# Performance work log

Measured on AMD Instinct MI355X. Metric: run time of the kernel, lower is better.

## Reference

```python
import jax, jax.numpy as jnp
import numpy as np
from jax.ops import segment_sum, segment_max

N, H, E, NEXP, K, L, HEADS, NM = 384, 768, 12288, 8, 2, 3, 4, 38
GAMMA, LAMBDA_SPD = 2.0, 0.5


def _ln(x, g, b, eps=1e-5):
    m = jnp.mean(x, -1, keepdims=True)
    v = jnp.mean((x - m) ** 2, -1, keepdims=True)
    return (x - m) / jnp.sqrt(v + eps) * g + b


def _gelu(x):
    return jax.nn.gelu(x, approximate=False)


def setup_inputs() -> dict:
    key = jax.random.key(0)
    ks = jax.random.split(key, 20)
    r = lambda i, sh: jax.random.normal(ks[i], sh, jnp.float32) * 0.02
    z = lambda sh: jnp.zeros(sh, jnp.float32)
    o = lambda sh: jnp.ones(sh, jnp.float32)
    return dict(
        feat_text=jax.random.normal(ks[0], (N, H), jnp.float32),
        feat_image=jax.random.normal(ks[1], (N, H), jnp.float32),
        spd_matrix=jax.random.uniform(ks[2], (N, N), dtype=jnp.float32),
        src=jax.random.randint(ks[3], (E,), 0, N, jnp.int32),
        dst=jax.random.randint(ks[4], (E,), 0, N, jnp.int32),
        mask_idx=jax.random.randint(ks[5], (NM,), 0, N, jnp.int32),
        mask_token=r(6, (H,)),
        gate_W=r(7, (H, NEXP)), gate_b=z((NEXP,)),
        exp_W1=r(8, (NEXP, H, H)), exp_b1=z((NEXP, H)),
        exp_g1=o((NEXP, H)), exp_be1=z((NEXP, H)),
        exp_W2=r(9, (NEXP, H, H)), exp_b2=z((NEXP, H)),
        gat_W=r(10, (L, H, HEADS * H)), gat_al=r(11, (L, HEADS, H)),
        gat_ar=r(12, (L, HEADS, H)), gat_b=z((L, HEADS * H)),
        dec_W1=r(13, (2, H, H)), dec_b1=z((2, H)),
        dec_g=o((2, H)), dec_be=z((2, H)),
        dec_W2=r(14, (2, H, H)), dec_b2=z((2, H)),
        spd_W1=r(15, (2 * H, H)), spd_b1=z((H,)),
        spd_g=o((H,)), spd_be=z((H,)),
        spd_W2=r(16, (H, 1)), spd_b2=z((1,)),
    )


def _forward(feat_text, feat_image, spd_matrix, mask_token, gate_W, gate_b,
             exp_W1, exp_b1, exp_g1, exp_be1, exp_W2, exp_b2,
             gat_W, gat_al, gat_ar, gat_b,
             dec_W1, dec_b1, dec_g, dec_be, dec_W2, dec_b2,
             spd_W1, spd_b1, spd_g, spd_be, spd_W2, spd_b2,
             src, dst, mask_idx):
    # mean of domain features, then mask-token replacement at fixed indices
    x = (feat_text + feat_image) * 0.5
    xm = x.at[mask_idx].set(mask_token)

    # --- MoE (all experts computed densely, top-2 gathered, as in source) ---
    gw = jax.nn.softmax(xm @ gate_W + gate_b, axis=-1)              # [N,NEXP]
    topw, topi = jax.lax.top_k(gw, K)
    topw = topw / jnp.sum(topw, -1, keepdims=True)
    eh = _gelu(_ln(jnp.einsum('nd,edh->neh', xm, exp_W1) + exp_b1, exp_g1, exp_be1))
    eo = jnp.einsum('neh,ehk->nek', eh, exp_W2) + exp_b2            # [N,NEXP,H]
    sel = jnp.take_along_axis(eo, topi[:, :, None], axis=1)          # [N,K,H]
    h = jnp.sum(sel * topw[:, :, None], axis=1)                      # [N,H]

    # --- stacked GATConv layers (DGL semantics), head-mean after each ---
    for l in range(L):
        f = (h @ gat_W[l]).reshape(N, HEADS, H)                      # [N,heads,H]
        el = jnp.sum(f * gat_al[l], -1)                              # [N,heads]
        er = jnp.sum(f * gat_ar[l], -1)
        e = jax.nn.leaky_relu(el[src] + er[dst], 0.2)                # [E,heads]
        emax = segment_max(e, dst, num_segments=N)
        emax = jnp.where(jnp.isfinite(emax), emax, 0.0)
        ex = jnp.exp(e - emax[dst])
        den = segment_sum(ex, dst, num_segments=N)
        alpha = ex / jnp.maximum(den[dst], 1e-9)                     # edge softmax by dst
        rst = segment_sum(alpha[:, :, None] * f[src], dst, num_segments=N)
        h = jnp.mean(rst + gat_b[l].reshape(HEADS, H), axis=1)       # [N,H]

    # --- domain reconstruction loss on masked nodes ---
    hm = h[mask_idx]
    feats = (feat_text, feat_image)
    recon = jnp.float32(0.0)
    for d in range(2):
        zz = _gelu(_ln(hm @ dec_W1[d] + dec_b1[d], dec_g[d], dec_be[d]))
        rec = zz @ dec_W2[d] + dec_b2[d]
        orig = feats[d][mask_idx]
        denom = jnp.maximum(jnp.linalg.norm(rec, axis=-1) * jnp.linalg.norm(orig, axis=-1), 1e-8)
        cos = jnp.sum(rec * orig, -1) / denom
        recon = recon + jnp.mean((1.0 - cos) ** GAMMA)

    # --- SPD loss over all N^2 pairs, vectorized ---
    # concat([h_i, h_j]) @ W1 == h_i @ W1[:H] + h_j @ W1[H:]  (exact decomposition)
    pa = h @ spd_W1[:H]                                              # [N,H]
    pb = h @ spd_W1[H:]                                              # [N,H]
    zp = _gelu(_ln(pa[:, None, :] + pb[None, :, :] + spd_b1, spd_g, spd_be))  # [N,N,H]
    pred = (zp @ spd_W2)[..., 0] + spd_b2[0]                         # [N,N]
    spd_loss = jnp.mean((pred - spd_matrix) ** 2)

    total = recon + LAMBDA_SPD * spd_loss
    return total, h


def reference(feat_text, feat_image, spd_matrix, src, dst, mask_idx, mask_token,
              gate_W, gate_b, exp_W1, exp_b1, exp_g1, exp_be1, exp_W2, exp_b2,
              gat_W, gat_al, gat_ar, gat_b,
              dec_W1, dec_b1, dec_g, dec_be, dec_W2, dec_b2,
              spd_W1, spd_b1, spd_g, spd_be, spd_W2, spd_b2):
    return _forward(feat_text, feat_image, spd_matrix, mask_token, gate_W, gate_b,
                    exp_W1, exp_b1, exp_g1, exp_be1, exp_W2, exp_b2,
                    gat_W, gat_al, gat_ar, gat_b,
                    dec_W1, dec_b1, dec_g, dec_be, dec_W2, dec_b2,
                    spd_W1, spd_b1, spd_g, spd_be, spd_W2, spd_b2,
                    src, dst, mask_idx)
```

## Files before the change

kernel.cpp:

```cpp
#include <hip/hip_runtime.h>
#include <hip/hip_bf16.h>
#include <math.h>

#define NN 384
#define HD 768
#define EE 12288
#define NCHUNK (EE / 256)
#define NEXPERT 8
#define TOPK 2
#define NLAYER 3
#define NHEADS 4
#define NMASK 38

typedef __attribute__((ext_vector_type(8))) short short8v;
typedef __attribute__((ext_vector_type(4))) float f32x4;
typedef __attribute__((ext_vector_type(2))) float f32x2;
typedef __attribute__((ext_vector_type(4))) int int4v;

__device__ __forceinline__ float gelu_f(float x) {
    return x * 0.5f * (1.f + erff(x * 0.70710678118654752440f));
}

__device__ __forceinline__ ushort f2bf(float x) {
    unsigned u = __float_as_uint(x);
    u += 0x7fffu + ((u >> 16) & 1u);
    return (ushort)(u >> 16);
}

__global__ __launch_bounds__(256) void k_xm_gate(const float* __restrict__ a,
        const float* __restrict__ b, const int* __restrict__ mask_idx,
        const float* __restrict__ mt, ushort* __restrict__ xm_bf,
        const float* __restrict__ gW, const float* __restrict__ gb,
        int* __restrict__ topi, float* __restrict__ topw) {
    int n = blockIdx.x, tid = threadIdx.x;
    __shared__ float xs[HD];
    __shared__ int ism;
    __shared__ float logits[NEXPERT];
    if (tid == 0) ism = 0;
    __syncthreads();
    if (tid < NMASK && mask_idx[tid] == n) ism = 1;
    __syncthreads();
#pragma unroll
    for (int r = 0; r < 3; r++) {
        int j = r * 256 + tid;
        float v = ism ? mt[j] : 0.5f * (a[(size_t)n * HD + j] + b[(size_t)n * HD + j]);
        xs[j] = v;
        xm_bf[(size_t)n * HD + j] = f2bf(v);
    }
    __syncthreads();
    int grp = tid >> 5;
    int l32 = tid & 31;
    float p = 0.f;
    for (int dd = l32; dd < HD; dd += 32) p += xs[dd] * gW[dd * NEXPERT + grp];
#pragma unroll
    for (int m = 1; m < 32; m <<= 1) p += __shfl_xor(p, m, 32);
    if (l32 == 0) logits[grp] = p + gb[grp];
    __syncthreads();
    if (tid == 0) {
        float mx = logits[0];
#pragma unroll
        for (int e = 1; e < NEXPERT; e++) mx = fmaxf(mx, logits[e]);
        float sm[NEXPERT]; float s = 0.f;
#pragma unroll
        for (int e = 0; e < NEXPERT; e++) { sm[e] = expf(logits[e] - mx); s += sm[e]; }
#pragma unroll
        for (int e = 0; e < NEXPERT; e++) sm[e] /= s;
        int i0 = 0; float b0 = sm[0];
#pragma unroll
        for (int e = 1; e < NEXPERT; e++) if (sm[e] > b0) { b0 = sm[e]; i0 = e; }
        int i1 = -1; float b1v = -1.f;
#pragma unroll
        for (int e = 0; e < NEXPERT; e++) if (e != i0 && sm[e] > b1v) { b1v = sm[e]; i1 = e; }
        float ssum = b0 + b1v;
        topi[n * 2] = i0; topi[n * 2 + 1] = i1;
        topw[n * 2] = b0 / ssum; topw[n * 2 + 1] = b1v / ssum;
    }
}

__global__ __launch_bounds__(256) void k_transpose_all(
        const float* __restrict__ w1, const float* __restrict__ w2,
        const float* __restrict__ gw, const float* __restrict__ sw,
        const float* __restrict__ dw1, const float* __restrict__ dw2,
        ushort* __restrict__ o1, ushort* __restrict__ o2, ushort* __restrict__ og,
        ushort* __restrict__ os, ushort* __restrict__ od1, ushort* __restrict__ od2) {
    int b = blockIdx.x;
    const float* src; ushort* dst; int N, loc, tilesX;
    if (b < 4608)       { src = w1;  dst = o1;  N = HD;     loc = b;         tilesX = 24; }
    else if (b < 9216)  { src = w2;  dst = o2;  N = HD;     loc = b - 4608;  tilesX = 24; }
    else if (b < 16128) { src = gw;  dst = og;  N = 4 * HD; loc = b - 9216;  tilesX = 96; }
    else if (b < 17280) { src = sw;  dst = os;  N = HD;     loc = b - 16128; tilesX = 24; }
    else if (b < 18432) { src = dw1; dst = od1; N = HD;     loc = b - 17280; tilesX = 24; }
    else                { src = dw2; dst = od2; N = HD;     loc = b - 18432; tilesX = 24; }
    const int K = HD;
    int tilesPerZ = tilesX * 24;
    int z = loc / tilesPerZ;
    int rem = loc - z * tilesPerZ;
    int ty = rem / tilesX, tx = rem - ty * tilesX;
    const float* inz = src + (size_t)z * K * N;
    ushort* outz = dst + (size_t)z * K * N;
    int n0 = tx * 32, k0 = ty * 32;

    __shared__ float t[32][36];
    int r = threadIdx.x >> 3, c4 = (threadIdx.x & 7) * 4;
    float4 v = *reinterpret_cast<const float4*>(inz + (size_t)(k0 + r) * N + n0 + c4);
    t[r][c4] = v.x; t[r][c4 + 1] = v.y; t[r][c4 + 2] = v.z; t[r][c4 + 3] = v.w;
    __syncthreads();
    int orow = n0 + r;
    uint2 p;
    ushort b0 = f2bf(t[c4 + 0][r]);
    ushort b1 = f2bf(t[c4 + 1][r]);
    ushort b2 = f2bf(t[c4 + 2][r]);
    ushort b3 = f2bf(t[c4 + 3][r]);
    p.x = (unsigned)b0 | ((unsigned)b1 << 16);
    p.y = (unsigned)b2 | ((unsigned)b3 << 16);
    *reinterpret_cast<uint2*>(outz + (size_t)orow * K + k0 + c4) = p;
}

__global__ __launch_bounds__(256) void k_moe_meta(const int* __restrict__ topi,
        int* __restrict__ ecnt, int* __restrict__ estart, int* __restrict__ posArr,
        int* __restrict__ eofpos, int* __restrict__ rowlist, int* __restrict__ dec_rs) {
    __shared__ int ti[NN * TOPK];
    __shared__ int cnt[NEXPERT];
    __shared__ int est[NEXPERT + 1];
    int tid = threadIdx.x;
    if (tid < NEXPERT) cnt[tid] = 0;
    __syncthreads();
    for (int a = tid; a < NN * TOPK; a += 256) ti[a] = topi[a];
    __syncthreads();
    for (int a = tid; a < NN * TOPK; a += 256) atomicAdd(&cnt[ti[a]], 1);
    __syncthreads();
    if (tid == 0) {
        int s = 0;
        for (int e = 0; e < NEXPERT; e++) { est[e] = s; s += cnt[e]; }
        est[NEXPERT] = s;
        dec_rs[0] = 0; dec_rs[1] = NMASK;
    }
    __syncthreads();
    if (tid < NEXPERT) { ecnt[tid] = cnt[tid]; estart[tid] = est[tid]; }
    if (tid == 0) estart[NEXPERT] = est[NEXPERT];
    for (int a = tid; a < NN * TOPK; a += 256) {
        int e = ti[a]; int rank = 0;
        for (int a2 = 0; a2 < a; a2++) rank += (ti[a2] == e) ? 1 : 0;
        int p = est[e] + rank;
        posArr[a] = p; eofpos[p] = e; rowlist[p] = a >> 1;
    }
}

__global__ __launch_bounds__(256) void k_hist(const int* __restrict__ dst,
                                              int* __restrict__ counts) {
    __shared__ int h[NN];
    int c = blockIdx.x;
    for (int i = threadIdx.x; i < NN; i += 256) h[i] = 0;
    __syncthreads();
    atomicAdd(&h[dst[c * 256 + threadIdx.x]], 1);
    __syncthreads();
    for (int i = threadIdx.x; i < NN; i += 256) counts[c * NN + i] = h[i];
}

__global__ __launch_bounds__(NN) void k_scan_all(const int* __restrict__ counts,
        int* __restrict__ chunkbase, int* __restrict__ nstart) {
    __shared__ int tot[NN];
    int n = threadIdx.x;
    int s = 0;
    for (int c = 0; c < NCHUNK; c++) { chunkbase[c * NN + n] = s; s += counts[c * NN + n]; }
    tot[n] = s;
    __syncthreads();
    for (int off = 1; off < NN; off <<= 1) {
        int v = tot[n];
        int add = (n >= off) ? tot[n - off] : 0;
        __syncthreads();
        tot[n] = v + add;
        __syncthreads();
    }
    nstart[n + 1] = tot[n];
    if (n == 0) nstart[0] = 0;
}

__global__ __launch_bounds__(256) void k_rank2(const int* __restrict__ dst,
        const int* __restrict__ chunkbase, const int* __restrict__ nstart,
        int* __restrict__ esorted) {
    __shared__ int ds[256];
    int c = blockIdx.x;
    int e = c * 256 + threadIdx.x;
    int d = dst[e];
    ds[threadIdx.x] = d;
    __syncthreads();
    int r = 0;
    for (int i = 0; i < threadIdx.x; i++) r += (ds[i] == d) ? 1 : 0;
    esorted[nstart[d] + chunkbase[c * NN + d] + r] = e;
}

__device__ __forceinline__ short8v ldfrag(const ushort* s, int r, int kb) {
    int c = kb ^ (r & 7);
    return *reinterpret_cast<const short8v*>(s + r * 64 + c * 8);
}

__global__ __launch_bounds__(256) void k_mfma_gemm(
        const ushort* __restrict__ A, const ushort* __restrict__ Bt, float* __restrict__ C,
        int M, int K, int lda, int ldc, long strideBt, long strideC,
        const int* __restrict__ rowsA, const int* __restrict__ Ms,
        const int* __restrict__ rowStarts) {
    int z = blockIdx.z;
    int Meff = Ms ? Ms[z] : M;
    int row0 = blockIdx.y * 64;
    if (row0 >= Meff) return;
    int col0 = blockIdx.x * 64;
    int rowbase = rowStarts ? rowStarts[z] : 0;
    const ushort* Btz = Bt + (size_t)z * strideBt;
    float* Cz = C + (size_t)rowbase * ldc + (size_t)z * strideC;
    const int* rz = rowsA ? (rowsA + rowbase) : nullptr;

    __shared__ ushort Asm[64 * 64];
    __shared__ ushort Bsm[64 * 64];

    int tid = threadIdx.x;
    int w = tid >> 6, lane = tid & 63;
    int wr = w >> 1, wc = w & 1;
    int l15 = lane & 15, lq = lane >> 4;

    f32x4 acc[2][2];
#pragma unroll
    for (int i = 0; i < 2; i++)
#pragma unroll
        for (int j = 0; j < 2; j++) acc[i][j] = (f32x4){0.f, 0.f, 0.f, 0.f};

    for (int k0 = 0; k0 < K; k0 += 64) {
#pragma unroll
        for (int ii = 0; ii < 2; ii++) {
            int i = tid + ii * 256;
            int r = i >> 3, c = i & 7;
            int cs = c ^ (r & 7);
            int4v av = (int4v){0, 0, 0, 0};
            int grow = row0 + r;
            if (grow < Meff) {
                int srow = rz ? rz[grow] : (rowbase + grow);
                av = *reinterpret_cast<const int4v*>(A + (size_t)srow * lda + k0 + c * 8);
            }
            *reinterpret_cast<int4v*>(&Asm[r * 64 + cs * 8]) = av;
            int4v bv = *reinterpret_cast<const int4v*>(Btz + (size_t)(col0 + r) * K + k0 + c * 8);
            *reinterpret_cast<int4v*>(&Bsm[r * 64 + cs * 8]) = bv;
        }
        __syncthreads();
#pragma unroll
        for (int ks = 0; ks < 2; ks++) {
            int kb = ks * 4 + lq;
            short8v a0 = ldfrag(Asm, wr * 32 + l15, kb);
            short8v a1 = ldfrag(Asm, wr * 32 + 16 + l15, kb);
            short8v b0 = ldfrag(Bsm, wc * 32 + l15, kb);
            short8v b1 = ldfrag(Bsm, wc * 32 + 16 + l15, kb);
            acc[0][0] = __builtin_amdgcn_mfma_f32_16x16x32_bf16(a0, b0, acc[0][0], 0, 0, 0);
            acc[0][1] = __builtin_amdgcn_mfma_f32_16x16x32_bf16(a0, b1, acc[0][1], 0, 0, 0);
            acc[1][0] = __builtin_amdgcn_mfma_f32_16x16x32_bf16(a1, b0, acc[1][0], 0, 0, 0);
            acc[1][1] = __builtin_amdgcn_mfma_f32_16x16x32_bf16(a1, b1, acc[1][1], 0, 0, 0);
        }
        __syncthreads();
    }
#pragma unroll
    for (int ai = 0; ai < 2; ai++)
#pragma unroll
        for (int bi = 0; bi < 2; bi++) {
            int rbase = row0 + wr * 32 + ai * 16 + (lq << 2);
            int cc = col0 + wc * 32 + bi * 16 + l15;
#pragma unroll
            for (int r = 0; r < 4; r++) {
                int rr = rbase + r;
                if (rr < Meff) Cz[(size_t)rr * ldc + cc] = acc[ai][bi][r];
            }
        }
}

__global__ __launch_bounds__(256) void k_ln_gelu(const float* __restrict__ t1,
        ushort* __restrict__ ehb, const float* __restrict__ b1, const float* __restrict__ g,
        const float* __restrict__ be, const int* __restrict__ eofpos) {
    int row = blockIdx.x;
    int e = eofpos[row];
    int tid = threadIdx.x;
    __shared__ float rA[4], rB[4];
    float v[3]; float s1 = 0.f, s2 = 0.f;
#pragma unroll
    for (int r = 0; r < 3; r++) {
        int c = r * 256 + tid;
        float x = t1[(size_t)row * HD + c] + b1[e * HD + c];
        v[r] = x; s1 += x; s2 += x * x;
    }
#pragma unroll
    for (int m = 1; m < 64; m <<= 1) { s1 += __shfl_xor(s1, m); s2 += __shfl_xor(s2, m); }
    int wave = tid >> 6, lane = tid & 63;
    if (lane == 0) { rA[wave] = s1; rB[wave] = s2; }
    __syncthreads();
    float S1 = rA[0] + rA[1] + rA[2] + rA[3];
    float S2 = rB[0] + rB[1] + rB[2] + rB[3];
    float mean = S1 * (1.f / HD);
    float var = S2 * (1.f / HD) - mean * mean;
    float rstd = rsqrtf(var + 1e-5f);
#pragma unroll
    for (int r = 0; r < 3; r++) {
        int c = r * 256 + tid;
        float zn = (v[r] - mean) * rstd * g[e * HD + c] + be[e * HD + c];
        ehb[(size_t)row * HD + c] = f2bf(gelu_f(zn));
    }
}

__global__ void k_combine_moe(const float* __restrict__ eo, const float* __restrict__ b2,
        const int* __restrict__ topi, const float* __restrict__ topw,
        const int* __restrict__ posArr, float* __restrict__ h, ushort* __restrict__ hb) {
    int n = blockIdx.x;
    int tid = threadIdx.x;
    int e0 = topi[n * 2], e1 = topi[n * 2 + 1];
    float w0 = topw[n * 2], w1 = topw[n * 2 + 1];
    int p0 = posArr[n * 2], p1 = posArr[n * 2 + 1];
    for (int j = tid; j < HD; j += 256) {
        float v0 = eo[(size_t)p0 * HD + j] + b2[e0 * HD + j];
        float v1 = eo[(size_t)p1 * HD + j] + b2[e1 * HD + j];
        float hv = w0 * v0 + w1 * v1;
        h[(size_t)n * HD + j] = hv;
        hb[(size_t)n * HD + j] = f2bf(hv);
    }
}

__global__ __launch_bounds__(256) void k_el_er(const float* __restrict__ f,
        const float* __restrict__ al, const float* __restrict__ ar,
        float* __restrict__ el, float* __restrict__ er) {
    int n = blockIdx.x;
    int hd = threadIdx.x >> 6, lane = threadIdx.x & 63;
    const float* fr = f + ((size_t)n * NHEADS + hd) * HD;
    float pl = 0.f, pr = 0.f;
    for (int j = lane; j < HD; j += 64) {
        float fv = fr[j];
        pl += fv * al[hd * HD + j];
        pr += fv * ar[hd * HD + j];
    }
#pragma unroll
    for (int m = 1; m < 64; m <<= 1) { pl += __shfl_xor(pl, m); pr += __shfl_xor(pr, m); }
    if (lane == 0) { el[n * NHEADS + hd] = pl; er[n * NHEADS + hd] = pr; }
}

__global__ __launch_bounds__(256) void k_gat_agg(const float* __restrict__ f,
        const float* __restrict__ el, const float* __restrict__ er,
        const int* __restrict__ src, const int* __restrict__ esorted,
        const int* __restrict__ nstart, const float* __restrict__ gb,
        float* __restrict__ hout, ushort* __restrict__ hb) {
    int n = blockIdx.x;
    int s0 = nstart[n], cnt = nstart[n + 1] - s0;
    int tid = threadIdx.x;
    __shared__ float red[4][NHEADS];
    __shared__ float emax_s[NHEADS], den_s[NHEADS];
    __shared__ float alpha_s[256][NHEADS];
    __shared__ int sn_s[256];
    float ern[NHEADS];
#pragma unroll
    for (int hd = 0; hd < NHEADS; hd++) ern[hd] = er[n * NHEADS + hd];
    int wave = tid >> 6, lane = tid & 63;

    float mx[NHEADS] = { -1e30f, -1e30f, -1e30f, -1e30f };
    for (int t = tid; t < cnt; t += 256) {
        int e = esorted[s0 + t]; int sn = src[e];
#pragma unroll
        for (int hd = 0; hd < NHEADS; hd++) {
            float v = el[sn * NHEADS + hd] + ern[hd];
            v = (v >= 0.f) ? v : 0.2f * v;
            mx[hd] = fmaxf(mx[hd], v);
        }
    }
#pragma unroll
    for (int hd = 0; hd < NHEADS; hd++) {
#pragma unroll
        for (int m = 1; m < 64; m <<= 1) mx[hd] = fmaxf(mx[hd], __shfl_xor(mx[hd], m));
    }
    if (lane == 0) { for (int hd = 0; hd < NHEADS; hd++) red[wave][hd] = mx[hd]; }
    __syncthreads();
    if (tid == 0) {
#pragma unroll
        for (int hd = 0; hd < NHEADS; hd++)
            emax_s[hd] = fmaxf(fmaxf(red[0][hd], red[1][hd]), fmaxf(red[2][hd], red[3][hd]));
    }
    __syncthreads();
    float sm[NHEADS] = { 0.f, 0.f, 0.f, 0.f };
    for (int t = tid; t < cnt; t += 256) {
        int e = esorted[s0 + t]; int sn = src[e];
#pragma unroll
        for (int hd = 0; hd < NHEADS; hd++) {
            float v = el[sn * NHEADS + hd] + ern[hd];
            v = (v >= 0.f) ? v : 0.2f * v;
            sm[hd] += expf(v - emax_s[hd]);
        }
    }
#pragma unroll
    for (int hd = 0; hd < NHEADS; hd++) {
#pragma unroll
        for (int m = 1; m < 64; m <<= 1) sm[hd] += __shfl_xor(sm[hd], m);
    }
    __syncthreads();
    if (lane == 0) { for (int hd = 0; hd < NHEADS; hd++) red[wave][hd] = sm[hd]; }
    __syncthreads();
    if (tid == 0) {
#pragma unroll
        for (int hd = 0; hd < NHEADS; hd++)
            den_s[hd] = red[0][hd] + red[1][hd] + red[2][hd] + red[3][hd];
    }
    __syncthreads();
    float acc[NHEADS][3] = {};
    for (int c0 = 0; c0 < cnt; c0 += 256) {
        int t = c0 + tid;
        if (t < cnt) {
            int e = esorted[s0 + t]; int sn = src[e];
            sn_s[tid] = sn;
#pragma unroll
            for (int hd = 0; hd < NHEADS; hd++) {
                float v = el[sn * NHEADS + hd] + ern[hd];
                v = (v >= 0.f) ? v : 0.2f * v;
                alpha_s[tid][hd] = expf(v - emax_s[hd]) / fmaxf(den_s[hd], 1e-9f);
            }
        }
        __syncthreads();
        int cm = cnt - c0; if (cm > 256) cm = 256;
        for (int i = 0; i < cm; i++) {
            int sn = sn_s[i];
            const float* fr = f + (size_t)sn * (NHEADS * HD);
#pragma unroll
            for (int hd = 0; hd < NHEADS; hd++) {
                float a = alpha_s[i][hd];
#pragma unroll
                for (int r = 0; r < 3; r++) acc[hd][r] += a * fr[hd * HD + r * 256 + tid];
            }
        }
        __syncthreads();
    }
#pragma unroll
    for (int r = 0; r < 3; r++) {
        int j = r * 256 + tid;
        float s = 0.f;
#pragma unroll
        for (int hd = 0; hd < NHEADS; hd++) s += acc[hd][r] + gb[hd * HD + j];
        float hv = 0.25f * s;
        hout[(size_t)n * HD + j] = hv;
        hb[(size_t)n * HD + j] = f2bf(hv);
    }
}

__global__ __launch_bounds__(256) void k_ln_gelu_dec(const float* __restrict__ t1,
        ushort* __restrict__ zzb, const float* __restrict__ b1, const float* __restrict__ g,
        const float* __restrict__ be) {
    int m = blockIdx.x, d = blockIdx.y;
    int row = d * NMASK + m;
    int tid = threadIdx.x;
    __shared__ float rA[4], rB[4];
    float v[3]; float s1 = 0.f, s2 = 0.f;
#pragma unroll
    for (int r = 0; r < 3; r++) {
        int c = r * 256 + tid;
        float x = t1[(size_t)row * HD + c] + b1[d * HD + c];
        v[r] = x; s1 += x; s2 += x * x;
    }
#pragma unroll
    for (int mm = 1; mm < 64; mm <<= 1) { s1 += __shfl_xor(s1, mm); s2 += __shfl_xor(s2, mm); }
    int wave = tid >> 6, lane = tid & 63;
    if (lane == 0) { rA[wave] = s1; rB[wave] = s2; }
    __syncthreads();
    float S1 = rA[0] + rA[1] + rA[2] + rA[3];
    float S2 = rB[0] + rB[1] + rB[2] + rB[3];
    float mean = S1 * (1.f / HD);
    float var = S2 * (1.f / HD) - mean * mean;
    float rstd = rsqrtf(var + 1e-5f);
#pragma unroll
    for (int r = 0; r < 3; r++) {
        int c = r * 256 + tid;
        float zn = (v[r] - mean) * rstd * g[d * HD + c] + be[d * HD + c];
        zzb[(size_t)row * HD + c] = f2bf(gelu_f(zn));
    }
}

__global__ __launch_bounds__(256) void k_cos(const float* __restrict__ rec,
        const float* __restrict__ b2, const int* __restrict__ mask_idx,
        const float* __restrict__ ft, const float* __restrict__ fi,
        float* __restrict__ rec_part) {
    int b = blockIdx.x;
    int d = b / NMASK, m = b % NMASK;
    int node = mask_idx[m];
    int tid = threadIdx.x;
    __shared__ float rA[4], rB[4], rC[4];
    const float* rrow = rec + (size_t)b * HD;
    const float* orig = (d == 0 ? ft : fi) + (size_t)node * HD;
    float pro = 0.f, prr = 0.f, poo = 0.f;
#pragma unroll
    for (int r = 0; r < 3; r++) {
        int c = r * 256 + tid;
        float rv = rrow[c] + b2[d * HD + c];
        float o = orig[c];
        pro += rv * o; prr += rv * rv; poo += o * o;
    }
#pragma unroll
    for (int mm = 1; mm < 64; mm <<= 1) {
        pro += __shfl_xor(pro, mm); prr += __shfl_xor(prr, mm); poo += __shfl_xor(poo, mm);
    }
    int wave = tid >> 6, lane = tid & 63;
    if (lane == 0) { rA[wave] = pro; rB[wave] = prr; rC[wave] = poo; }
    __syncthreads();
    if (tid == 0) {
        float P = rA[0] + rA[1] + rA[2] + rA[3];
        float R = rB[0] + rB[1] + rB[2] + rB[3];
        float O = rC[0] + rC[1] + rC[2] + rC[3];
        float denom = fmaxf(sqrtf(R) * sqrtf(O), 1e-8f);
        float cosv = P / denom;
        float t = 1.f - cosv;
        rec_part[b] = (t * t) * (1.f / (float)NMASK);
    }
}

__global__ __launch_bounds__(256) void k_spd_prep(float* __restrict__ pab,
        const float* __restrict__ b1, ushort* __restrict__ pp_bf,
        float* __restrict__ Svec, float* __restrict__ Qvec) {
    int r = blockIdx.x, tid = threadIdx.x;
    bool isA = r < NN;
    float* row = pab + (size_t)r * HD;
    __shared__ float rA[4], rB[4];
    float vv[3]; float s1 = 0.f, s2 = 0.f;
#pragma unroll
    for (int rr = 0; rr < 3; rr++) {
        int j = rr * 256 + tid;
        float v = row[j];
        if (isA) v += b1[j];
        vv[rr] = v; s1 += v; s2 += v * v;
    }
#pragma unroll
    for (int m = 1; m < 64; m <<= 1) { s1 += __shfl_xor(s1, m); s2 += __shfl_xor(s2, m); }
    int wave = tid >> 6, lane = tid & 63;
    if (lane == 0) { rA[wave] = s1; rB[wave] = s2; }
#pragma unroll
    for (int rr = 0; rr < 3; rr++) {
        int j = rr * 256 + tid;
        if (isA) row[j] = vv[rr];
        pp_bf[(size_t)r * HD + j] = f2bf(vv[rr]);
    }
    __syncthreads();
    if (tid == 0) {
        Svec[r] = rA[0] + rA[1] + rA[2] + rA[3];
        Qvec[r] = rB[0] + rB[1] + rB[2] + rB[3];
    }
}

#define GC1 2.3022085f
#define GC2 0.10294429f
__global__ __launch_bounds__(256) void k_spd2(const float* __restrict__ pab,
        const float* __restrict__ Svec, const float* __restrict__ Qvec,
        const float* __restrict__ cross, const float* __restrict__ g,
        const float* __restrict__ be, const float* __restrict__ w2,
        const float* __restrict__ b2, const float* __restrict__ spd,
        float* __restrict__ partials) {
    __shared__ float wsum[4];
    int i = blockIdx.x;
    int wave = threadIdx.x >> 6, lane = threadIdx.x & 63;
    const f32x2* paP = reinterpret_cast<const f32x2*>(pab + (size_t)i * HD);
    const f32x2* gP = reinterpret_cast<const f32x2*>(g);
    const f32x2* beP = reinterpret_cast<const f32x2*>(be);
    const f32x2* w2P = reinterpret_cast<const f32x2*>(w2);
    f32x2 pa2[6], g2[6], be2[6], w22[6];
#pragma unroll
    for (int r = 0; r < 6; r++) {
        int e = r * 64 + lane;
        pa2[r] = paP[e];
        g2[r] = gP[e];
        be2[r] = beP[e];
        w22[r] = w2P[e];
    }
    float Sa = Svec[i], Qa = Qvec[i];
    float bacc = 0.f;
    float b2v = b2[0];
    for (int j = blockIdx.y * 4 + wave; j < NN; j += 32) {
        const f32x2* pbj = reinterpret_cast<const f32x2*>(pab + (size_t)(NN + j) * HD);
        float mean = (Sa + Svec[NN + j]) * (1.f / HD);
        float ex2 = (Qa + Qvec[NN + j] + 2.f * cross[(size_t)i * NN + j]) * (1.f / HD);
        float var = ex2 - mean * mean;
        float rstd = rsqrtf(var + 1e-5f);
        f32x2 rstd2 = (f32x2){rstd, rstd};
        float nmr = -mean * rstd;
        f32x2 nmr2 = (f32x2){nmr, nmr};
        f32x2 dot2 = (f32x2){0.f, 0.f};
#pragma unroll
        for (int r = 0; r < 6; r++) {
            f32x2 z = pa2[r] + pbj[r * 64 + lane];
            f32x2 u = z * rstd2 + nmr2;
            f32x2 zn = u * g2[r] + be2[r];
            f32x2 t2 = zn * zn;
            f32x2 p = t2 * (f32x2){GC2, GC2} + (f32x2){GC1, GC1};
            f32x2 ua = zn * p;
            float e0 = __builtin_amdgcn_exp2f(-ua.x);
            float e1 = __builtin_amdgcn_exp2f(-ua.y);
            f32x2 rr = (f32x2){__builtin_amdgcn_rcpf(1.f + e0),
                               __builtin_amdgcn_rcpf(1.f + e1)};
            f32x2 gl = zn * rr;
            dot2 = gl * w22[r] + dot2;
        }
        float dot = dot2.x + dot2.y;
#pragma unroll
        for (int m = 1; m < 64; m <<= 1) dot += __shfl_xor(dot, m);
        if (lane == 0) {
            float d = (dot + b2v) - spd[(size_t)i * NN + j];
            bacc += d * d;
        }
    }
    if (lane == 0) wsum[wave] = bacc;
    __syncthreads();
    if (threadIdx.x == 0) partials[i * 8 + blockIdx.y] = wsum[0] + wsum[1] + wsum[2] + wsum[3];
}

__global__ __launch_bounds__(256) void k_out(const float* __restrict__ h,
        const float* __restrict__ rec_part, const float* __restrict__ spd_part,
        float* __restrict__ out) {
    if (blockIdx.x < NN * HD / 256) {
        int i = blockIdx.x * 256 + threadIdx.x;
        out[1 + i] = h[i];
        return;
    }
    __shared__ float rA[4], rB[4];
    int tid = threadIdx.x;
    float sp = 0.f, rc = 0.f;
    for (int t = tid; t < 8 * NN; t += 256) sp += spd_part[t];
    for (int t = tid; t < 2 * NMASK; t += 256) rc += rec_part[t];
#pragma unroll
    for (int m = 1; m < 64; m <<= 1) { sp += __shfl_xor(sp, m); rc += __shfl_xor(rc, m); }
    int wave = tid >> 6, lane = tid & 63;
    if (lane == 0) { rA[wave] = sp; rB[wave] = rc; }
    __syncthreads();
    if (tid == 0) {
        float SP = rA[0] + rA[1] + rA[2] + rA[3];
        float RC = rB[0] + rB[1] + rB[2] + rB[3];
        out[0] = RC + 0.5f * (SP * (1.f / ((float)NN * (float)NN)));
    }
}

extern "C" void kernel_launch(void* const* d_in, const int* in_sizes, int n_in,
                              void* d_out, int out_size, void* d_ws, size_t ws_size,
                              hipStream_t stream) {
    const float* feat_text = (const float*)d_in[0];
    const float* feat_image = (const float*)d_in[1];
    const float* spd_matrix = (const float*)d_in[2];
    const int*   src       = (const int*)d_in[3];
    const int*   dst       = (const int*)d_in[4];
    const int*   mask_idx  = (const int*)d_in[5];
    const float* mask_token = (const float*)d_in[6];
    const float* gate_W = (const float*)d_in[7];
    const float* gate_b = (const float*)d_in[8];
    const float* exp_W1 = (const float*)d_in[9];
    const float* exp_b1 = (const float*)d_in[10];
    const float* exp_g1 = (const float*)d_in[11];
    const float* exp_be1 = (const float*)d_in[12];
    const float* exp_W2 = (const float*)d_in[13];
    const float* exp_b2 = (const float*)d_in[14];
    const float* gat_W  = (const float*)d_in[15];
    const float* gat_al = (const float*)d_in[16];
    const float* gat_ar = (const float*)d_in[17];
    const float* gat_b  = (const float*)d_in[18];
    const float* dec_W1 = (const float*)d_in[19];
    const float* dec_b1 = (const float*)d_in[20];
    const float* dec_g  = (const float*)d_in[21];
    const float* dec_be = (const float*)d_in[22];
    const float* dec_W2 = (const float*)d_in[23];
    const float* dec_b2 = (const float*)d_in[24];
    const float* spd_W1 = (const float*)d_in[25];
    const float* spd_b1 = (const float*)d_in[26];
    const float* spd_g  = (const float*)d_in[27];
    const float* spd_be = (const float*)d_in[28];
    const float* spd_W2 = (const float*)d_in[29];
    const float* spd_b2 = (const float*)d_in[30];
    (void)in_sizes; (void)n_in; (void)ws_size; (void)out_size;

    float* ws = (float*)d_ws;
    size_t off = 0;
    auto alloc = [&](size_t nfl) { float* p = ws + off; off += (nfl + 3) & ~(size_t)3; return p; };
    float* hA   = alloc((size_t)NN * HD);
    float* hB   = alloc((size_t)NN * HD);
    float* t1   = alloc((size_t)NN * TOPK * HD);
    float* eo   = alloc((size_t)NN * TOPK * HD);
    float* fbuf = alloc((size_t)NN * NHEADS * HD);
    float* el   = alloc(NN * NHEADS);
    float* er   = alloc(NN * NHEADS);
    float* pab  = alloc((size_t)2 * NN * HD);
    float* cross = alloc((size_t)NN * NN);
    float* Svec = alloc(2 * NN);
    float* Qvec = alloc(2 * NN);
    float* topw = alloc(NN * TOPK);
    float* rec_part = alloc(2 * NMASK + 4);
    float* spd_part = alloc(8 * NN);
    int* topi    = (int*)alloc(NN * TOPK);
    int* ecnt    = (int*)alloc(16);
    int* estart  = (int*)alloc(16);
    int* posArr  = (int*)alloc(NN * TOPK);
    int* eofpos  = (int*)alloc(NN * TOPK);
    int* rowlist = (int*)alloc(NN * TOPK);
    int* dec_rs  = (int*)alloc(4);
    int* nstart  = (int*)alloc(NN + 4);
    int* esorted = (int*)alloc(EE);
    int* counts    = (int*)alloc((size_t)NCHUNK * NN);
    int* chunkbase = (int*)alloc((size_t)NCHUNK * NN);
    ushort* xm_bf  = (ushort*)alloc((size_t)NN * HD / 2);
    ushort* eh_bf  = (ushort*)alloc((size_t)NN * TOPK * HD / 2);
    ushort* hA_bf  = (ushort*)alloc((size_t)NN * HD / 2);
    ushort* hB_bf  = (ushort*)alloc((size_t)NN * HD / 2);
    ushort* pp_bf  = (ushort*)alloc((size_t)2 * NN * HD / 2);
    ushort* expW1t = (ushort*)alloc((size_t)NEXPERT * HD * HD / 2);
    ushort* expW2t = (ushort*)alloc((size_t)NEXPERT * HD * HD / 2);
    ushort* gatWt  = (ushort*)alloc((size_t)NLAYER * NHEADS * HD * HD / 2);
    ushort* spdW1t = (ushort*)alloc((size_t)2 * HD * HD / 2);
    ushort* decW1t = (ushort*)alloc((size_t)2 * HD * HD / 2);
    ushort* decW2t = (ushort*)alloc((size_t)2 * HD * HD / 2);

    k_transpose_all<<<dim3(19584), dim3(256), 0, stream>>>(
        exp_W1, exp_W2, gat_W, spd_W1, dec_W1, dec_W2,
        expW1t, expW2t, gatWt, spdW1t, decW1t, decW2t);

    k_xm_gate<<<dim3(NN), dim3(256), 0, stream>>>(
        feat_text, feat_image, mask_idx, mask_token, xm_bf, gate_W, gate_b, topi, topw);
    k_moe_meta<<<dim3(1), dim3(256), 0, stream>>>(topi, ecnt, estart, posArr, eofpos,
                                                  rowlist, dec_rs);

    k_hist<<<dim3(NCHUNK), dim3(256), 0, stream>>>(dst, counts);
    k_scan_all<<<dim3(1), dim3(NN), 0, stream>>>(counts, chunkbase, nstart);
    k_rank2<<<dim3(NCHUNK), dim3(256), 0, stream>>>(dst, chunkbase, nstart, esorted);

    k_mfma_gemm<<<dim3(HD / 64, 12, NEXPERT), dim3(256), 0, stream>>>(
        xm_bf, expW1t, t1, 0, HD, HD, HD, (long)HD * HD, 0, rowlist, ecnt, estart);
    k_ln_gelu<<<dim3(NN * TOPK), dim3(256), 0, stream>>>(t1, eh_bf, exp_b1, exp_g1, exp_be1, eofpos);
    k_mfma_gemm<<<dim3(HD / 64, 12, NEXPERT), dim3(256), 0, stream>>>(
        eh_bf, expW2t, eo, 0, HD, HD, HD, (long)HD * HD, 0, nullptr, ecnt, estart);
    k_combine_moe<<<dim3(NN), dim3(256), 0, stream>>>(eo, exp_b2, topi, topw, posArr, hA, hA_bf);

    float* hcur = hA; float* hnxt = hB;
    ushort* hcur_bf = hA_bf; ushort* hnxt_bf = hB_bf;
    for (int l = 0; l < NLAYER; l++) {
        k_mfma_gemm<<<dim3(NHEADS * HD / 64, NN / 64, 1), dim3(256), 0, stream>>>(
            hcur_bf, gatWt + (size_t)l * NHEADS * HD * HD, fbuf,
            NN, HD, HD, NHEADS * HD, 0, 0, nullptr, nullptr, nullptr);
        k_el_er<<<dim3(NN), dim3(256), 0, stream>>>(
            fbuf, gat_al + (size_t)l * NHEADS * HD, gat_ar + (size_t)l * NHEADS * HD, el, er);
        k_gat_agg<<<dim3(NN), dim3(256), 0, stream>>>(
            fbuf, el, er, src, esorted, nstart, gat_b + (size_t)l * NHEADS * HD, hnxt, hnxt_bf);
        float* t = hcur; hcur = hnxt; hnxt = t;
        ushort* tb = hcur_bf; hcur_bf = hnxt_bf; hnxt_bf = tb;
    }

    k_mfma_gemm<<<dim3(HD / 64, 1, 2), dim3(256), 0, stream>>>(
        hcur_bf, decW1t, t1, NMASK, HD, HD, HD, (long)HD * HD, (long)NMASK * HD,
        mask_idx, nullptr, nullptr);
    k_ln_gelu_dec<<<dim3(NMASK, 2), dim3(256), 0, stream>>>(t1, eh_bf, dec_b1, dec_g, dec_be);
    k_mfma_gemm<<<dim3(HD / 64, 1, 2), dim3(256), 0, stream>>>(
        eh_bf, decW2t, eo, NMASK, HD, HD, HD, (long)HD * HD, 0,
        nullptr, nullptr, dec_rs);
    k_cos<<<dim3(2 * NMASK), dim3(256), 0, stream>>>(
        eo, dec_b2, mask_idx, feat_text, feat_image, rec_part);

    k_mfma_gemm<<<dim3(HD / 64, NN / 64, 2), dim3(256), 0, stream>>>(
        hcur_bf, spdW1t, pab, NN, HD, HD, HD, (long)HD * HD, (long)NN * HD,
        nullptr, nullptr, nullptr);
    k_spd_prep<<<dim3(2 * NN), dim3(256), 0, stream>>>(pab, spd_b1, pp_bf, Svec, Qvec);
    k_mfma_gemm<<<dim3(NN / 64, NN / 64, 1), dim3(256), 0, stream>>>(
        pp_bf, pp_bf + (size_t)NN * HD, cross, NN, HD, HD, NN, 0, 0,
        nullptr, nullptr, nullptr);
    k_spd2<<<dim3(NN, 8), dim3(256), 0, stream>>>(
        pab, Svec, Qvec, cross, spd_g, spd_be, spd_W2, spd_b2, spd_matrix, spd_part);

    k_out<<<dim3(NN * HD / 256 + 1), dim3(256), 0, stream>>>(
        hcur, rec_part, spd_part, (float*)d_out);
}
```

Measured before the change: 364.8 us.

## Restructure SPD pair kernel to single-wave blocks processing four j columns at once

The SPD pairwise kernel now launches one wave per block over a 384x32 grid instead of four waves over 384x8. Each wave handles four j columns together, sharing the register-resident pa/g/be/w2 values and interleaving four independent GELU chains to expose more instruction-level parallelism. The LDS reduction and barrier go away, the partials buffer grows to 32 per row, and the final reduction reads more partials. The four scalar accumulators and replaced packed f32x2 math raise register use.

Result: no change. 370.1 us (+1.5%).

```diff
diff --git a/kernel.cpp b/kernel.cpp
--- a/kernel.cpp
+++ b/kernel.cpp
@@ -14,7 +14,6 @@
 
 typedef __attribute__((ext_vector_type(8))) short short8v;
 typedef __attribute__((ext_vector_type(4))) float f32x4;
-typedef __attribute__((ext_vector_type(2))) float f32x2;
 typedef __attribute__((ext_vector_type(4))) int int4v;
 
 __device__ __forceinline__ float gelu_f(float x) {
@@ -541,67 +540,90 @@
 
 #define GC1 2.3022085f
 #define GC2 0.10294429f
-__global__ __launch_bounds__(256) void k_spd2(const float* __restrict__ pab,
+__global__ __launch_bounds__(64) void k_spd2(const float* __restrict__ pab,
         const float* __restrict__ Svec, const float* __restrict__ Qvec,
         const float* __restrict__ cross, const float* __restrict__ g,
         const float* __restrict__ be, const float* __restrict__ w2,
         const float* __restrict__ b2, const float* __restrict__ spd,
         float* __restrict__ partials) {
-    __shared__ float wsum[4];
-    int i = blockIdx.x;
-    int wave = threadIdx.x >> 6, lane = threadIdx.x & 63;
-    const f32x2* paP = reinterpret_cast<const f32x2*>(pab + (size_t)i * HD);
-    const f32x2* gP = reinterpret_cast<const f32x2*>(g);
-    const f32x2* beP = reinterpret_cast<const f32x2*>(be);
-    const f32x2* w2P = reinterpret_cast<const f32x2*>(w2);
-    f32x2 pa2[6], g2[6], be2[6], w22[6];
-#pragma unroll
-    for (int r = 0; r < 6; r++) {
+    int i = blockIdx.x, y = blockIdx.y, lane = threadIdx.x;
+    const float* paP = pab + (size_t)i * HD;
+    float pa_r[12], g_r[12], be_r[12], w2_r[12];
+#pragma unroll
+    for (int r = 0; r < 12; r++) {
         int e = r * 64 + lane;
-        pa2[r] = paP[e];
-        g2[r] = gP[e];
-        be2[r] = beP[e];
-        w22[r] = w2P[e];
+        pa_r[r] = paP[e];
+        g_r[r] = g[e];
+        be_r[r] = be[e];
+        w2_r[r] = w2[e];
+    }
+#pragma unroll
+    for (int r = 0; r < 12; r++) {
+        asm volatile("" : "+v"(pa_r[r]), "+v"(g_r[r]), "+v"(be_r[r]), "+v"(w2_r[r]));
     }
     float Sa = Svec[i], Qa = Qvec[i];
+    float b2v = b2[0];
     float bacc = 0.f;
-    float b2v = b2[0];
-    for (int j = blockIdx.y * 4 + wave; j < NN; j += 32) {
-        const f32x2* pbj = reinterpret_cast<const f32x2*>(pab + (size_t)(NN + j) * HD);
-        float mean = (Sa + Svec[NN + j]) * (1.f / HD);
-        float ex2 = (Qa + Qvec[NN + j] + 2.f * cross[(size_t)i * NN + j]) * (1.f / HD);
-        float var = ex2 - mean * mean;
-        float rstd = rsqrtf(var + 1e-5f);
-        f32x2 rstd2 = (f32x2){rstd, rstd};
-        float nmr = -mean * rstd;
-        f32x2 nmr2 = (f32x2){nmr, nmr};
-        f32x2 dot2 = (f32x2){0.f, 0.f};
-#pragma unroll
-        for (int r = 0; r < 6; r++) {
-            f32x2 z = pa2[r] + pbj[r * 64 + lane];
-            f32x2 u = z * rstd2 + nmr2;
-            f32x2 zn = u * g2[r] + be2[r];
-            f32x2 t2 = zn * zn;
-            f32x2 p = t2 * (f32x2){GC2, GC2} + (f32x2){GC1, GC1};
-            f32x2 ua = zn * p;
-            float e0 = __builtin_amdgcn_exp2f(-ua.x);
-            float e1 = __builtin_amdgcn_exp2f(-ua.y);
-            f32x2 rr = (f32x2){__builtin_amdgcn_rcpf(1.f + e0),
-                               __builtin_amdgcn_rcpf(1.f + e1)};
-            f32x2 gl = zn * rr;
-            dot2 = gl * w22[r] + dot2;
-        }
-        float dot = dot2.x + dot2.y;
-#pragma unroll
-        for (int m = 1; m < 64; m <<= 1) dot += __shfl_xor(dot, m);
+#pragma unroll
+    for (int t = 0; t < 3; t++) {
+        int j0 = y + t * 128;
+        const float* pb[4];
+        float rstd[4], nmr[4];
+#pragma unroll
+        for (int u = 0; u < 4; u++) {
+            int j = j0 + u * 32;
+            pb[u] = pab + (size_t)(NN + j) * HD;
+            float mean = (Sa + Svec[NN + j]) * (1.f / HD);
+            float ex2 = (Qa + Qvec[NN + j] + 2.f * cross[(size_t)i * NN + j]) * (1.f / HD);
+            float var = ex2 - mean * mean;
+            float rs = rsqrtf(var + 1e-5f);
+            rstd[u] = rs; nmr[u] = -mean * rs;
+        }
+        float dt0 = 0.f, dt1 = 0.f, dt2 = 0.f, dt3 = 0.f;
+#pragma unroll
+        for (int r = 0; r < 12; r++) {
+            int e = r * 64 + lane;
+            float z0 = pa_r[r] + pb[0][e];
+            float z1 = pa_r[r] + pb[1][e];
+            float z2 = pa_r[r] + pb[2][e];
+            float z3 = pa_r[r] + pb[3][e];
+            float zn0 = fmaf(fmaf(z0, rstd[0], nmr[0]), g_r[r], be_r[r]);
+            float zn1 = fmaf(fmaf(z1, rstd[1], nmr[1]), g_r[r], be_r[r]);
+            float zn2 = fmaf(fmaf(z2, rstd[2], nmr[2]), g_r[r], be_r[r]);
+            float zn3 = fmaf(fmaf(z3, rstd[3], nmr[3]), g_r[r], be_r[r]);
+            float ua0 = zn0 * fmaf(zn0 * zn0, GC2, GC1);
+            float ua1 = zn1 * fmaf(zn1 * zn1, GC2, GC1);
+            float ua2 = zn2 * fmaf(zn2 * zn2, GC2, GC1);
+            float ua3 = zn3 * fmaf(zn3 * zn3, GC2, GC1);
+            float e0 = __builtin_amdgcn_exp2f(-ua0);
+            float e1 = __builtin_amdgcn_exp2f(-ua1);
+            float e2 = __builtin_amdgcn_exp2f(-ua2);
+            float e3 = __builtin_amdgcn_exp2f(-ua3);
+            float gl0 = zn0 * __builtin_amdgcn_rcpf(1.f + e0);
+            float gl1 = zn1 * __builtin_amdgcn_rcpf(1.f + e1);
+            float gl2 = zn2 * __builtin_amdgcn_rcpf(1.f + e2);
+            float gl3 = zn3 * __builtin_amdgcn_rcpf(1.f + e3);
+            dt0 = fmaf(gl0, w2_r[r], dt0);
+            dt1 = fmaf(gl1, w2_r[r], dt1);
+            dt2 = fmaf(gl2, w2_r[r], dt2);
+            dt3 = fmaf(gl3, w2_r[r], dt3);
+        }
+#pragma unroll
+        for (int m = 1; m < 64; m <<= 1) {
+            dt0 += __shfl_xor(dt0, m);
+            dt1 += __shfl_xor(dt1, m);
+            dt2 += __shfl_xor(dt2, m);
+            dt3 += __shfl_xor(dt3, m);
+        }
         if (lane == 0) {
-            float d = (dot + b2v) - spd[(size_t)i * NN + j];
-            bacc += d * d;
-        }
-    }
-    if (lane == 0) wsum[wave] = bacc;
-    __syncthreads();
-    if (threadIdx.x == 0) partials[i * 8 + blockIdx.y] = wsum[0] + wsum[1] + wsum[2] + wsum[3];
+            float d0 = (dt0 + b2v) - spd[(size_t)i * NN + j0];
+            float d1 = (dt1 + b2v) - spd[(size_t)i * NN + j0 + 32];
+            float d2 = (dt2 + b2v) - spd[(size_t)i * NN + j0 + 64];
+            float d3 = (dt3 + b2v) - spd[(size_t)i * NN + j0 + 96];
+            bacc += d0 * d0 + d1 * d1 + d2 * d2 + d3 * d3;
+        }
+    }
+    if (lane == 0) partials[i * 32 + y] = bacc;
 }
 
 __global__ __launch_bounds__(256) void k_out(const float* __restrict__ h,
@@ -615,7 +637,7 @@
     __shared__ float rA[4], rB[4];
     int tid = threadIdx.x;
     float sp = 0.f, rc = 0.f;
-    for (int t = tid; t < 8 * NN; t += 256) sp += spd_part[t];
+    for (int t = tid; t < 32 * NN; t += 256) sp += spd_part[t];
     for (int t = tid; t < 2 * NMASK; t += 256) rc += rec_part[t];
 #pragma unroll
     for (int m = 1; m < 64; m <<= 1) { sp += __shfl_xor(sp, m); rc += __shfl_xor(rc, m); }
@@ -681,7 +703,7 @@
     float* Qvec = alloc(2 * NN);
     float* topw = alloc(NN * TOPK);
     float* rec_part = alloc(2 * NMASK + 4);
-    float* spd_part = alloc(8 * NN);
+    float* spd_part = alloc(32 * NN);
     int* topi    = (int*)alloc(NN * TOPK);
     int* ecnt    = (int*)alloc(16);
     int* estart  = (int*)alloc(16);
@@ -756,7 +778,7 @@
     k_mfma_gemm<<<dim3(NN / 64, NN / 64, 1), dim3(256), 0, stream>>>(
         pp_bf, pp_bf + (size_t)NN * HD, cross, NN, HD, HD, NN, 0, 0,
         nullptr, nullptr, nullptr);
-    k_spd2<<<dim3(NN, 8), dim3(256), 0, stream>>>(
+    k_spd2<<<dim3(NN, 32), dim3(64), 0, stream>>>(
         pab, Svec, Qvec, cross, spd_g, spd_be, spd_W2, spd_b2, spd_matrix, spd_part);
 
     k_out<<<dim3(NN * HD / 256 + 1), dim3(256), 0, stream>>>(
```
